# Optimization experiments

Measured on AMD Instinct MI355X. Metric: run time of the kernel, lower is better.

## Reference

```python
import jax, jax.numpy as jnp
import numpy as np

E = 262144   # num edges
T = 1048576  # num triplets
H = 128      # hidden_channels
IE = 64      # int_emb_size
NR = 6       # num_radial
NS = 7       # num_spherical
BD = 8       # basis_emb_size_dist
BA = 8       # basis_emb_size_angle


def setup_inputs() -> dict:
    key = jax.random.key(0)
    ks = jax.random.split(key, 32)
    def rnd(k, shape, s=0.1):
        return jax.random.normal(k, shape, dtype=jnp.float32) * s
    return {
        "x1": rnd(ks[0], (T, H), 1.0),
        "x_old": rnd(ks[1], (E, H), 1.0),
        "rbf0": rnd(ks[2], (E, NR), 1.0),
        "sbf": rnd(ks[3], (T, NS * NR), 1.0),
        "idx_kj": jax.random.randint(ks[4], (T,), 0, E),
        "idx_ji": jax.random.randint(ks[5], (T,), 0, E),
        "W_rbf1": rnd(ks[6], (NR, BD)),
        "W_rbf2": rnd(ks[7], (BD, H)),
        "W_sbf1": rnd(ks[8], (NS * NR, BA)),
        "W_sbf2": rnd(ks[9], (BA, IE)),
        "W_rbf": rnd(ks[10], (NR, H)),
        "W_kj": rnd(ks[11], (H, H)), "b_kj": rnd(ks[12], (H,)),
        "W_ji": rnd(ks[13], (H, H)), "b_ji": rnd(ks[14], (H,)),
        "W_connect": rnd(ks[15], (H, H)), "b_connect": rnd(ks[16], (H,)),
        "W_get_up": rnd(ks[17], (H, H)), "b_get_up": rnd(ks[18], (H,)),
        "W_down": rnd(ks[19], (H, IE)), "b_down": rnd(ks[20], (IE,)),
        "W_up": rnd(ks[21], (IE, H)), "b_up": rnd(ks[22], (H,)),
        "res_before_W": rnd(ks[23], (1, 2, H, H)), "res_before_b": rnd(ks[24], (1, 2, H)),
        "W_lin": rnd(ks[25], (H, H)), "b_lin": rnd(ks[26], (H,)),
        "res_after_W": rnd(ks[27], (2, 2, H, H)), "res_after_b": rnd(ks[28], (2, 2, H)),
    }


def _residual(x, W, b):
    # x + act(lin2(act(lin1(x))))
    h = jax.nn.silu(x @ W[0] + b[0])
    return x + jax.nn.silu(h @ W[1] + b[1])


def reference(x1, x_old, rbf0, sbf, idx_kj, idx_ji, W_rbf1, W_rbf2, W_sbf1, W_sbf2,
              W_rbf, W_kj, b_kj, W_ji, b_ji, W_connect, b_connect, W_get_up, b_get_up,
              W_down, b_down, W_up, b_up, res_before_W, res_before_b, W_lin, b_lin,
              res_after_W, res_after_b):
    act = jax.nn.silu  # swish
    nE = x_old.shape[0]
    # aggregate plane features onto edges
    x_up = jax.ops.segment_sum(x1, idx_ji, num_segments=nE)
    x_up = act(x_up @ W_get_up + b_get_up)
    x_ji = act(x_old @ W_ji + b_ji)
    x_kj = act(x_old @ W_kj + b_kj)
    rbf = (rbf0 @ W_rbf1) @ W_rbf2            # [E, H]
    x_kj = x_kj * rbf
    x_kj = act(x_kj @ W_down + b_down)        # [E, IE]
    sbf_p = (sbf @ W_sbf1) @ W_sbf2           # [T, IE]
    x_kj = x_kj[idx_kj] * sbf_p               # gather edges -> triplets
    x_kj = jax.ops.segment_sum(x_kj, idx_ji, num_segments=nE)  # scatter back to edges
    x_kj = act(x_kj @ W_up + b_up)
    e1 = x_ji + x_kj
    e1 = act(e1 @ W_connect + b_connect) + x_up
    for i in range(res_before_W.shape[0]):
        e1 = _residual(e1, res_before_W[i], res_before_b[i])
    e1 = act(e1 @ W_lin + b_lin) + x_old
    for i in range(res_after_W.shape[0]):
        e1 = _residual(e1, res_after_W[i], res_after_b[i])
    e2 = (rbf0 @ W_rbf) * e1
    return (e1, e2)
```

## Files before the change

### kernel.cpp

```cpp
#include <hip/hip_runtime.h>

#define E_N 262144
#define T_N 1048576

typedef short  bf16x8  __attribute__((ext_vector_type(8)));
typedef short  bf16x4v __attribute__((ext_vector_type(4)));
typedef float  f32x4   __attribute__((ext_vector_type(4)));

#define OFF_KJ    0
#define OFF_DOWN  16384
#define OFF_UP    24576
#define OFF_JI    32768
#define OFF_GU    49152
#define OFF_CN    65536
#define OFF_RB0   81920
#define OFF_RB1   98304
#define OFF_LIN   114688
#define OFF_RA00  131072
#define OFF_RA01  147456
#define OFF_RA10  163840
#define OFF_RA11  180224
#define OFF_END   196608
#define WREG_BYTES 524288u

#define OFFB_AGG   0u
#define OFFB_XKJ   33554432u
#define OFFB_WREG  67108864u
#define OFFB_CNT   67633152u
#define OFFB_POS   68683776u
#define OFFB_TRI   69732352u
#define OFFB_BS    73926656u
#define OFFB_BP    73927680u

__device__ __forceinline__ float silu_f(float x) { return x / (1.0f + __expf(-x)); }

__device__ __forceinline__ unsigned short f2bf(float f) {
  union { float f; unsigned int u; } v; v.f = f;
  unsigned int u = v.u;
  return (unsigned short)((u + 0x7fffu + ((u >> 16) & 1u)) >> 16);
}
__device__ __forceinline__ float bf2f(unsigned short h) {
  union { unsigned int u; float f; } v; v.u = ((unsigned int)h) << 16;
  return v.f;
}

template<int NC>
__device__ __forceinline__ void stage_tile(const float* __restrict__ g, char* __restrict__ lds) {
  constexpr int RB = NC * 2;
  constexpr int C4 = NC / 4;
  for (int i = threadIdx.x; i < 64 * C4; i += 512) {
    int r = i / C4, c4 = i % C4;
    float4 v = *(const float4*)(g + (size_t)r * NC + c4 * 4);
    bf16x4v h;
    h[0] = (short)f2bf(v.x); h[1] = (short)f2bf(v.y);
    h[2] = (short)f2bf(v.z); h[3] = (short)f2bf(v.w);
    *(bf16x4v*)(lds + r * RB + ((c4 * 8) ^ ((r & 7) << 4))) = h;
  }
}

__device__ __forceinline__ void stage_tile_bf16_64(const unsigned short* __restrict__ g,
                                                   char* __restrict__ lds) {
  int i = threadIdx.x;
  int r = i >> 3, c = i & 7;
  int4 v = *(const int4*)((const char*)g + r * 128 + c * 16);
  *(int4*)(lds + r * 128 + ((c * 16) ^ ((r & 7) << 4))) = v;
}

template<int MREP, int NREP, int KSTEPS, int RB>
__device__ __forceinline__ void mfma_gemm(const char* __restrict__ lds, int row0, int col0,
                                          const unsigned short* __restrict__ WT, int lane,
                                          f32x4 (&acc)[MREP][NREP]) {
  const int kg = lane >> 4, r15 = lane & 15;
#pragma unroll
  for (int m = 0; m < MREP; ++m)
#pragma unroll
    for (int n = 0; n < NREP; ++n) acc[m][n] = (f32x4){0.f, 0.f, 0.f, 0.f};
#pragma unroll
  for (int kk = 0; kk < KSTEPS; ++kk) {
    bf16x8 a[MREP], bfr[NREP];
#pragma unroll
    for (int m = 0; m < MREP; ++m) {
      int row = row0 + m * 16 + r15;
      a[m] = *(const bf16x8*)(lds + row * RB + ((kk * 64 + kg * 16) ^ ((row & 7) << 4)));
    }
#pragma unroll
    for (int n = 0; n < NREP; ++n) {
      int nc = col0 + n * 16 + r15;
      bfr[n] = *(const bf16x8*)((const short*)WT + nc * (KSTEPS * 32) + kk * 32 + kg * 8);
    }
#pragma unroll
    for (int m = 0; m < MREP; ++m)
#pragma unroll
      for (int n = 0; n < NREP; ++n)
        acc[m][n] = __builtin_amdgcn_mfma_f32_16x16x32_bf16(a[m], bfr[n], acc[m][n], 0, 0, 0);
  }
}

template<int RB>
__device__ __forceinline__ void write_cd(char* __restrict__ lds, int wrow, int wcol, int lane,
                                         const f32x4 (&v)[2][2]) {
  const int kg = lane >> 4, r15 = lane & 15;
#pragma unroll
  for (int m = 0; m < 2; ++m)
#pragma unroll
    for (int n = 0; n < 2; ++n)
#pragma unroll
      for (int r = 0; r < 4; ++r) {
        int row = wrow + m * 16 + kg * 4 + r;
        int col = wcol + n * 16 + r15;
        *(unsigned short*)(lds + row * RB + ((col * 2) ^ ((row & 7) << 4))) = f2bf(v[m][n][r]);
      }
}

__global__ void __launch_bounds__(256) k_prep(
    const float* __restrict__ W_kj, const float* __restrict__ W_down,
    const float* __restrict__ W_up, const float* __restrict__ W_ji,
    const float* __restrict__ W_get_up, const float* __restrict__ W_connect,
    const float* __restrict__ rbW, const float* __restrict__ W_lin,
    const float* __restrict__ raW,
    const float* __restrict__ W_rbf1, const float* __restrict__ W_rbf2,
    unsigned short* __restrict__ wreg) {
  int b = blockIdx.x;
  if (b == 13) {
    float* W12 = (float*)(wreg + OFF_END);
    for (int i = threadIdx.x; i < 768; i += 256) {
      int r = i >> 7, n = i & 127;
      float s = 0.f;
#pragma unroll
      for (int q = 0; q < 8; ++q) s += W_rbf1[r * 8 + q] * W_rbf2[q * 128 + n];
      W12[i] = s;
    }
    return;
  }
  const float* src; int K = 128, N = 128; int off;
  switch (b) {
    case 0:  src = W_kj;          off = OFF_KJ;  break;
    case 1:  src = W_down;        off = OFF_DOWN; N = 64;  break;
    case 2:  src = W_up;          off = OFF_UP;   K = 64;  break;
    case 3:  src = W_ji;          off = OFF_JI;  break;
    case 4:  src = W_get_up;      off = OFF_GU;  break;
    case 5:  src = W_connect;     off = OFF_CN;  break;
    case 6:  src = rbW;           off = OFF_RB0; break;
    case 7:  src = rbW + 16384;   off = OFF_RB1; break;
    case 8:  src = W_lin;         off = OFF_LIN; break;
    case 9:  src = raW;           off = OFF_RA00; break;
    case 10: src = raW + 16384;   off = OFF_RA01; break;
    case 11: src = raW + 32768;   off = OFF_RA10; break;
    default: src = raW + 49152;   off = OFF_RA11; break;
  }
  unsigned short* dst = wreg + off;
  for (int i = threadIdx.x; i < K * N; i += 256) {
    int k = i / N, n = i % N;
    dst[n * K + k] = f2bf(src[i]);
  }
}

__global__ void __launch_bounds__(256) k_hist(const int* __restrict__ idx_ji,
                                              int* __restrict__ counts) {
  int t = blockIdx.x * 256 + threadIdx.x;
  atomicAdd(&counts[idx_ji[t]], 1);
}

__global__ void __launch_bounds__(1024) k_scan1(const int* __restrict__ counts,
                                                int* __restrict__ locpre,
                                                int* __restrict__ bsum) {
  __shared__ int s[1024];
  int i = blockIdx.x * 1024 + threadIdx.x;
  int v = counts[i];
  s[threadIdx.x] = v; __syncthreads();
  for (int o = 1; o < 1024; o <<= 1) {
    int t = (threadIdx.x >= o) ? s[threadIdx.x - o] : 0;
    __syncthreads();
    s[threadIdx.x] += t;
    __syncthreads();
  }
  locpre[i] = s[threadIdx.x] - v;
  if (threadIdx.x == 1023) bsum[blockIdx.x] = s[1023];
}

__global__ void __launch_bounds__(256) k_scan2(const int* __restrict__ bsum,
                                               int* __restrict__ bpre, int* __restrict__ offs) {
  __shared__ int s[256];
  int v = bsum[threadIdx.x];
  s[threadIdx.x] = v; __syncthreads();
  for (int o = 1; o < 256; o <<= 1) {
    int t = (threadIdx.x >= o) ? s[threadIdx.x - o] : 0;
    __syncthreads();
    s[threadIdx.x] += t;
    __syncthreads();
  }
  bpre[threadIdx.x] = s[threadIdx.x] - v;
  if (threadIdx.x == 0) offs[E_N] = T_N;
}

__global__ void __launch_bounds__(1024) k_scan3(const int* __restrict__ locpre,
                                                const int* __restrict__ bpre,
                                                int* __restrict__ offs,
                                                int* __restrict__ pos) {
  int i = blockIdx.x * 1024 + threadIdx.x;
  int v = locpre[i] + bpre[blockIdx.x];
  offs[i] = v;
  pos[i] = v;
}

__global__ void __launch_bounds__(256) k_fill(const int* __restrict__ idx_ji,
                                              int* __restrict__ pos, int* __restrict__ tri) {
  int t = blockIdx.x * 256 + threadIdx.x;
  int e = idx_ji[t];
  int slot = atomicAdd(&pos[e], 1);
  tri[slot] = t;
}

__global__ void __launch_bounds__(256) k_sbfp(const float* __restrict__ sbf,
                                              const float* __restrict__ W_sbf1,
                                              const float* __restrict__ W_sbf2,
                                              unsigned int* __restrict__ sbfp) {
  __shared__ float s_s[8][42];
  __shared__ float s_t8[8][8];
  int t0 = blockIdx.x * 8;
  for (int i = threadIdx.x; i < 8 * 42; i += 256)
    s_s[i / 42][i % 42] = sbf[(size_t)t0 * 42 + i];
  __syncthreads();
  if (threadIdx.x < 64) {
    int w8 = threadIdx.x >> 3, bb = threadIdx.x & 7;
    float s = 0.f;
#pragma unroll
    for (int r = 0; r < 42; ++r) s += s_s[w8][r] * W_sbf1[r * 8 + bb];
    s_t8[w8][bb] = s;
  }
  __syncthreads();
  int w8 = threadIdx.x >> 5, jj = threadIdx.x & 31;
  float sp0 = 0.f, sp1 = 0.f;
#pragma unroll
  for (int bb = 0; bb < 8; ++bb) {
    float tv = s_t8[w8][bb];
    sp0 += tv * W_sbf2[bb * 64 + jj * 2];
    sp1 += tv * W_sbf2[bb * 64 + jj * 2 + 1];
  }
  unsigned int u = (unsigned int)f2bf(sp0) | ((unsigned int)f2bf(sp1) << 16);
  sbfp[(size_t)(t0 + w8) * 32 + jj] = u;
}

__global__ void __launch_bounds__(256) k_aggB(const int* __restrict__ offs,
                                              const int* __restrict__ tri,
                                              const int* __restrict__ idx_kj,
                                              const unsigned int* __restrict__ sbfp,
                                              const unsigned int* __restrict__ xkj,
                                              unsigned int* __restrict__ agg) {
  int sub = threadIdx.x >> 5, jj = threadIdx.x & 31;
  int e = blockIdx.x * 8 + sub;
  int o0 = offs[e], o1 = offs[e + 1];
  float a0 = 0.f, a1 = 0.f;
  for (int i = o0; i < o1; ++i) {
    int t = tri[i];
    int kj = idx_kj[t];
    unsigned int sv = sbfp[(size_t)t * 32 + jj];
    unsigned int xv = xkj[(size_t)kj * 32 + jj];
    a0 += bf2f((unsigned short)(sv & 0xffff)) * bf2f((unsigned short)(xv & 0xffff));
    a1 += bf2f((unsigned short)(sv >> 16)) * bf2f((unsigned short)(xv >> 16));
  }
  agg[(size_t)e * 32 + jj] = (unsigned int)f2bf(a0) | ((unsigned int)f2bf(a1) << 16);
}

__global__ void __launch_bounds__(256) k_xupg(const int* __restrict__ offs,
                                              const int* __restrict__ tri,
                                              const float* __restrict__ x1,
                                              float* __restrict__ out) {
  int sub = threadIdx.x >> 6, h2 = threadIdx.x & 63;
  int e = blockIdx.x * 4 + sub;
  int o0 = offs[e], o1 = offs[e + 1];
  float a0 = 0.f, a1 = 0.f;
  for (int i = o0; i < o1; ++i) {
    int t = tri[i];
    float2 v = *(const float2*)(x1 + (size_t)t * 128 + h2 * 2);
    a0 += v.x; a1 += v.y;
  }
  *(float2*)(out + (size_t)e * 128 + h2 * 2) = make_float2(a0, a1);
}

__global__ void __launch_bounds__(512, 4) phaseA(
    const float* __restrict__ x_old, const float* __restrict__ rbf0,
    const unsigned short* __restrict__ wreg,
    const float* __restrict__ b_kj, const float* __restrict__ b_down,
    unsigned short* __restrict__ xkjdown) {
  __shared__ char lds[32768];
  char* B0 = lds;
  char* B1 = lds + 16384;
  const int tid = threadIdx.x, lane = tid & 63, wave = tid >> 6;
  const int kg = lane >> 4, r15 = lane & 15;
  const int wrow = (wave >> 2) * 32, wcol = (wave & 3) * 32;
  const size_t e_base = (size_t)blockIdx.x * 64;
  const float* W12 = (const float*)(wreg + OFF_END);

  stage_tile<128>(x_old + e_base * 128, B0);
  __syncthreads();

  f32x4 acc[2][2], val[2][2];
  mfma_gemm<2, 2, 4, 256>(B0, wrow, wcol, wreg + OFF_KJ, lane, acc);
#pragma unroll
  for (int n = 0; n < 2; ++n) {
    int col = wcol + n * 16 + r15;
    float bk = b_kj[col];
    float wc[6];
#pragma unroll
    for (int q = 0; q < 6; ++q) wc[q] = W12[q * 128 + col];
#pragma unroll
    for (int m = 0; m < 2; ++m)
#pragma unroll
      for (int r = 0; r < 4; ++r) {
        int row = wrow + m * 16 + kg * 4 + r;
        const float* rp = rbf0 + (e_base + row) * 6;
        float rv = rp[0]*wc[0] + rp[1]*wc[1] + rp[2]*wc[2] + rp[3]*wc[3] + rp[4]*wc[4] + rp[5]*wc[5];
        val[m][n][r] = silu_f(acc[m][n][r] + bk) * rv;
      }
  }
  __syncthreads();
  write_cd<256>(B1, wrow, wcol, lane, val);
  __syncthreads();

  const int wrow2 = (wave >> 1) * 16, wcol2 = (wave & 1) * 32;
  f32x4 a2[1][2];
  mfma_gemm<1, 2, 4, 256>(B1, wrow2, wcol2, wreg + OFF_DOWN, lane, a2);
#pragma unroll
  for (int n = 0; n < 2; ++n) {
    int col = wcol2 + n * 16 + r15;
    float bd = b_down[col];
#pragma unroll
    for (int r = 0; r < 4; ++r) {
      int row = wrow2 + kg * 4 + r;
      xkjdown[(e_base + row) * 64 + col] = f2bf(silu_f(a2[0][n][r] + bd));
    }
  }
}

__global__ void __launch_bounds__(512, 4) phaseC1(
    const float* __restrict__ x_old, float* __restrict__ e1buf,
    const unsigned short* __restrict__ agg, const unsigned short* __restrict__ wreg,
    const float* __restrict__ b_up, const float* __restrict__ b_ji,
    const float* __restrict__ b_get_up, const float* __restrict__ b_connect,
    const float* __restrict__ rbB, const float* __restrict__ b_lin,
    const float* __restrict__ raB,
    const float* __restrict__ rbf0, const float* __restrict__ W_rbf,
    float* __restrict__ e2o) {
  __shared__ char lds[32768];
  char* B0 = lds;
  char* B1 = lds + 16384;
  const int tid = threadIdx.x, lane = tid & 63, wave = tid >> 6;
  const int kg = lane >> 4, r15 = lane & 15;
  const int wrow = (wave >> 2) * 32, wcol = (wave & 3) * 32;
  const size_t e_base = (size_t)blockIdx.x * 64;

  stage_tile_bf16_64(agg + e_base * 64, B0);
  stage_tile<128>(x_old + e_base * 128, B1);
  __syncthreads();

  f32x4 acc[2][2], acc2[2][2], keep[2][2], tmp[2][2];

  mfma_gemm<2, 2, 2, 128>(B0, wrow, wcol, wreg + OFF_UP, lane, acc);
  mfma_gemm<2, 2, 4, 256>(B1, wrow, wcol, wreg + OFF_JI, lane, acc2);
#pragma unroll
  for (int n = 0; n < 2; ++n) {
    int col = wcol + n * 16 + r15;
    float bu = b_up[col], bj = b_ji[col];
#pragma unroll
    for (int m = 0; m < 2; ++m)
#pragma unroll
      for (int r = 0; r < 4; ++r)
        keep[m][n][r] = silu_f(acc2[m][n][r] + bj) + silu_f(acc[m][n][r] + bu);
  }
  __syncthreads();
  write_cd<256>(B0, wrow, wcol, lane, keep);
  stage_tile<128>(e1buf + e_base * 128, B1);
  __syncthreads();

  mfma_gemm<2, 2, 4, 256>(B1, wrow, wcol, wreg + OFF_GU, lane, acc);
  mfma_gemm<2, 2, 4, 256>(B0, wrow, wcol, wreg + OFF_CN, lane, acc2);
#pragma unroll
  for (int n = 0; n < 2; ++n) {
    int col = wcol + n * 16 + r15;
    float bg = b_get_up[col], bc = b_connect[col];
#pragma unroll
    for (int m = 0; m < 2; ++m)
#pragma unroll
      for (int r = 0; r < 4; ++r)
        keep[m][n][r] = silu_f(acc2[m][n][r] + bc) + silu_f(acc[m][n][r] + bg);
  }
  __syncthreads();
  write_cd<256>(B1, wrow, wcol, lane, keep);
  __syncthreads();

  mfma_gemm<2, 2, 4, 256>(B1, wrow, wcol, wreg + OFF_RB0, lane, acc);
#pragma unroll
  for (int n = 0; n < 2; ++n) {
    float b0v = rbB[wcol + n * 16 + r15];
#pragma unroll
    for (int m = 0; m < 2; ++m)
#pragma unroll
      for (int r = 0; r < 4; ++r) tmp[m][n][r] = silu_f(acc[m][n][r] + b0v);
  }
  __syncthreads();
  write_cd<256>(B0, wrow, wcol, lane, tmp);
  __syncthreads();

  mfma_gemm<2, 2, 4, 256>(B0, wrow, wcol, wreg + OFF_RB1, lane, acc);
#pragma unroll
  for (int n = 0; n < 2; ++n) {
    float b1v = rbB[128 + wcol + n * 16 + r15];
#pragma unroll
    for (int m = 0; m < 2; ++m)
#pragma unroll
      for (int r = 0; r < 4; ++r) keep[m][n][r] += silu_f(acc[m][n][r] + b1v);
  }
  __syncthreads();
  write_cd<256>(B1, wrow, wcol, lane, keep);
  __syncthreads();

  mfma_gemm<2, 2, 4, 256>(B1, wrow, wcol, wreg + OFF_LIN, lane, acc);
#pragma unroll
  for (int n = 0; n < 2; ++n) {
    int col = wcol + n * 16 + r15;
    float bl = b_lin[col];
#pragma unroll
    for (int m = 0; m < 2; ++m)
#pragma unroll
      for (int r = 0; r < 4; ++r) {
        int row = wrow + m * 16 + kg * 4 + r;
        keep[m][n][r] = silu_f(acc[m][n][r] + bl) + x_old[(e_base + row) * 128 + col];
      }
  }
  __syncthreads();
  write_cd<256>(B0, wrow, wcol, lane, keep);
  __syncthreads();

  mfma_gemm<2, 2, 4, 256>(B0, wrow, wcol, wreg + OFF_RA00, lane, acc);
#pragma unroll
  for (int n = 0; n < 2; ++n) {
    float bv = raB[wcol + n * 16 + r15];
#pragma unroll
    for (int m = 0; m < 2; ++m)
#pragma unroll
      for (int r = 0; r < 4; ++r) tmp[m][n][r] = silu_f(acc[m][n][r] + bv);
  }
  __syncthreads();
  write_cd<256>(B1, wrow, wcol, lane, tmp);
  __syncthreads();

  mfma_gemm<2, 2, 4, 256>(B1, wrow, wcol, wreg + OFF_RA01, lane, acc);
#pragma unroll
  for (int n = 0; n < 2; ++n) {
    float bv = raB[128 + wcol + n * 16 + r15];
#pragma unroll
    for (int m = 0; m < 2; ++m)
#pragma unroll
      for (int r = 0; r < 4; ++r) keep[m][n][r] += silu_f(acc[m][n][r] + bv);
  }
  __syncthreads();
  write_cd<256>(B0, wrow, wcol, lane, keep);
  __syncthreads();

  mfma_gemm<2, 2, 4, 256>(B0, wrow, wcol, wreg + OFF_RA10, lane, acc);
#pragma unroll
  for (int n = 0; n < 2; ++n) {
    float bv = raB[256 + wcol + n * 16 + r15];
#pragma unroll
    for (int m = 0; m < 2; ++m)
#pragma unroll
      for (int r = 0; r < 4; ++r) tmp[m][n][r] = silu_f(acc[m][n][r] + bv);
  }
  __syncthreads();
  write_cd<256>(B1, wrow, wcol, lane, tmp);
  __syncthreads();

  mfma_gemm<2, 2, 4, 256>(B1, wrow, wcol, wreg + OFF_RA11, lane, acc);
#pragma unroll
  for (int n = 0; n < 2; ++n) {
    int col = wcol + n * 16 + r15;
    float bv = raB[384 + col];
    float wc[6];
#pragma unroll
    for (int q = 0; q < 6; ++q) wc[q] = W_rbf[q * 128 + col];
#pragma unroll
    for (int m = 0; m < 2; ++m)
#pragma unroll
      for (int r = 0; r < 4; ++r) {
        int row = wrow + m * 16 + kg * 4 + r;
        size_t e = e_base + row;
        float val = keep[m][n][r] + silu_f(acc[m][n][r] + bv);
        e1buf[e * 128 + col] = val;
        if (e2o) {
          const float* rp = rbf0 + e * 6;
          float rv = rp[0]*wc[0] + rp[1]*wc[1] + rp[2]*wc[2] + rp[3]*wc[3] + rp[4]*wc[4] + rp[5]*wc[5];
          e2o[e * 128 + col] = val * rv;
        }
      }
  }
}

__global__ void __launch_bounds__(256) k_e2(const float* __restrict__ e1,
                                            const float* __restrict__ rbf0,
                                            const float* __restrict__ W_rbf,
                                            float* __restrict__ e2) {
  size_t gid = (size_t)blockIdx.x * 256 + threadIdx.x;
  int e = (int)(gid >> 5);
  int c = (int)(gid & 31) << 2;
  float r6[6];
#pragma unroll
  for (int r = 0; r < 6; ++r) r6[r] = rbf0[(size_t)e * 6 + r];
  float4 v = *(const float4*)(e1 + (size_t)e * 128 + c);
  float4 o;
  float rv;
  rv = 0.f;
#pragma unroll
  for (int r = 0; r < 6; ++r) rv += r6[r] * W_rbf[r * 128 + c + 0];
  o.x = v.x * rv;
  rv = 0.f;
#pragma unroll
  for (int r = 0; r < 6; ++r) rv += r6[r] * W_rbf[r * 128 + c + 1];
  o.y = v.y * rv;
  rv = 0.f;
#pragma unroll
  for (int r = 0; r < 6; ++r) rv += r6[r] * W_rbf[r * 128 + c + 2];
  o.z = v.z * rv;
  rv = 0.f;
#pragma unroll
  for (int r = 0; r < 6; ++r) rv += r6[r] * W_rbf[r * 128 + c + 3];
  o.w = v.w * rv;
  *(float4*)(e2 + (size_t)e * 128 + c) = o;
}

extern "C" void kernel_launch(void* const* d_in, const int* in_sizes, int n_in,
                              void* d_out, int out_size, void* d_ws, size_t ws_size,
                              hipStream_t stream) {
  const float* x1        = (const float*)d_in[0];
  const float* x_old     = (const float*)d_in[1];
  const float* rbf0      = (const float*)d_in[2];
  const float* sbf       = (const float*)d_in[3];
  const int*   idx_kj    = (const int*)d_in[4];
  const int*   idx_ji    = (const int*)d_in[5];
  const float* W_rbf1    = (const float*)d_in[6];
  const float* W_rbf2    = (const float*)d_in[7];
  const float* W_sbf1    = (const float*)d_in[8];
  const float* W_sbf2    = (const float*)d_in[9];
  const float* W_rbf     = (const float*)d_in[10];
  const float* W_kj      = (const float*)d_in[11];
  const float* b_kj      = (const float*)d_in[12];
  const float* W_ji      = (const float*)d_in[13];
  const float* b_ji      = (const float*)d_in[14];
  const float* W_connect = (const float*)d_in[15];
  const float* b_connect = (const float*)d_in[16];
  const float* W_get_up  = (const float*)d_in[17];
  const float* b_get_up  = (const float*)d_in[18];
  const float* W_down    = (const float*)d_in[19];
  const float* b_down    = (const float*)d_in[20];
  const float* W_up      = (const float*)d_in[21];
  const float* b_up      = (const float*)d_in[22];
  const float* rbW       = (const float*)d_in[23];
  const float* rbB       = (const float*)d_in[24];
  const float* W_lin     = (const float*)d_in[25];
  const float* b_lin     = (const float*)d_in[26];
  const float* raW       = (const float*)d_in[27];
  const float* raB       = (const float*)d_in[28];

  float* e1buf = (float*)d_out;
  char*  base2 = (char*)d_out + (size_t)E_N * 128 * 4;
  float* e2out = (float*)base2;

  unsigned short* xkj_b = (unsigned short*)(base2 + OFFB_XKJ);
  int* counts = (int*)(base2 + OFFB_CNT);
  int* pos    = (int*)(base2 + OFFB_POS);
  int* tri    = (int*)(base2 + OFFB_TRI);
  int* bsum   = (int*)(base2 + OFFB_BS);
  int* bpre   = (int*)(base2 + OFFB_BP);

  const size_t need_ws = (size_t)WREG_BYTES + (size_t)E_N * 64 * 2;
  const bool fuse = ws_size >= need_ws;
  unsigned short* wreg  = fuse ? (unsigned short*)d_ws
                               : (unsigned short*)(base2 + OFFB_WREG);
  unsigned short* agg_b = fuse ? (unsigned short*)((char*)d_ws + WREG_BYTES)
                               : (unsigned short*)(base2 + OFFB_AGG);

  unsigned int* sbfp_u = (unsigned int*)e1buf;

  k_prep<<<14, 256, 0, stream>>>(W_kj, W_down, W_up, W_ji, W_get_up, W_connect,
                                 rbW, W_lin, raW, W_rbf1, W_rbf2, wreg);

  hipMemsetAsync(counts, 0, (E_N + 1) * sizeof(int), stream);
  k_hist<<<T_N / 256, 256, 0, stream>>>(idx_ji, counts);
  k_scan1<<<256, 1024, 0, stream>>>(counts, pos, bsum);
  k_scan2<<<1, 256, 0, stream>>>(bsum, bpre, counts);
  k_scan3<<<256, 1024, 0, stream>>>(pos, bpre, counts, pos);
  k_fill<<<T_N / 256, 256, 0, stream>>>(idx_ji, pos, tri);

  k_sbfp<<<T_N / 8, 256, 0, stream>>>(sbf, W_sbf1, W_sbf2, sbfp_u);

  phaseA<<<E_N / 64, 512, 0, stream>>>(x_old, rbf0, wreg, b_kj, b_down, xkj_b);

  k_aggB<<<E_N / 8, 256, 0, stream>>>(counts, tri, idx_kj, sbfp_u,
                                      (const unsigned int*)xkj_b, (unsigned int*)agg_b);

  k_xupg<<<E_N / 4, 256, 0, stream>>>(counts, tri, x1, e1buf);

  phaseC1<<<E_N / 64, 512, 0, stream>>>(x_old, e1buf, agg_b, wreg,
                                        b_up, b_ji, b_get_up, b_connect, rbB, b_lin, raB,
                                        rbf0, W_rbf, fuse ? e2out : nullptr);
  if (!fuse)
    k_e2<<<E_N * 32 / 256, 256, 0, stream>>>(e1buf, rbf0, W_rbf, e2out);
}
```

Before: 1.356 ms.

## Restructure edge MLP chain as per-wave register-resident transposed GEMMs

Replaces the 512-thread phaseC1 kernel with phaseC2, in which each wave owns 16 edges and computes every layer as W^T·X^T. Activations stay in registers and are repacked to bf16 through a small per-wave LDS scratch area, so the block-wide __syncthreads between layers go away. Weights are read straight from global memory as MFMA A operands instead of being staged, and bf16 conversion uses v_cvt_pk_bf16_f32. Weight reads now go through cache on every layer, and register pressure rises with 8 fragments of keep and h.

```diff
diff --git a/kernel.cpp b/kernel.cpp
--- a/kernel.cpp
+++ b/kernel.cpp
@@ -34,6 +34,13 @@
 
 __device__ __forceinline__ float silu_f(float x) { return x / (1.0f + __expf(-x)); }
 
+__device__ __forceinline__ f32x4 silu4(f32x4 v) {
+  f32x4 r;
+#pragma unroll
+  for (int i = 0; i < 4; ++i) r[i] = silu_f(v[i]);
+  return r;
+}
+
 __device__ __forceinline__ unsigned short f2bf(float f) {
   union { float f; unsigned int u; } v; v.f = f;
   unsigned int u = v.u;
@@ -42,6 +49,19 @@
 __device__ __forceinline__ float bf2f(unsigned short h) {
   union { unsigned int u; float f; } v; v.u = ((unsigned int)h) << 16;
   return v.f;
+}
+
+__device__ __forceinline__ unsigned cvtpk(float lo, float hi) {
+  unsigned r;
+  asm("v_cvt_pk_bf16_f32 %0, %1, %2" : "=v"(r) : "v"(lo), "v"(hi));
+  return r;
+}
+
+__device__ __forceinline__ bf16x8 pack8(f32x4 a, f32x4 b) {
+  union { bf16x8 v; unsigned u[4]; } t;
+  t.u[0] = cvtpk(a[0], a[1]); t.u[1] = cvtpk(a[2], a[3]);
+  t.u[2] = cvtpk(b[0], b[1]); t.u[3] = cvtpk(b[2], b[3]);
+  return t.v;
 }
 
 template<int NC>
@@ -56,14 +76,6 @@
     h[2] = (short)f2bf(v.z); h[3] = (short)f2bf(v.w);
     *(bf16x4v*)(lds + r * RB + ((c4 * 8) ^ ((r & 7) << 4))) = h;
   }
-}
-
-__device__ __forceinline__ void stage_tile_bf16_64(const unsigned short* __restrict__ g,
-                                                   char* __restrict__ lds) {
-  int i = threadIdx.x;
-  int r = i >> 3, c = i & 7;
-  int4 v = *(const int4*)((const char*)g + r * 128 + c * 16);
-  *(int4*)(lds + r * 128 + ((c * 16) ^ ((r & 7) << 4))) = v;
 }
 
 template<int MREP, int NREP, int KSTEPS, int RB>
@@ -333,7 +345,40 @@
   }
 }
 
-__global__ void __launch_bounds__(512, 4) phaseC1(
+
+__device__ __forceinline__ void repack(const f32x4 (&v)[8], char* __restrict__ rowp,
+                                       int kg, int sw, bf16x8 (&B)[4]) {
+  asm volatile("s_waitcnt lgkmcnt(0)" ::: "memory");
+#pragma unroll
+  for (int f = 0; f < 8; ++f) {
+    uint2 u;
+    u.x = cvtpk(v[f][0], v[f][1]);
+    u.y = cvtpk(v[f][2], v[f][3]);
+    *(uint2*)(rowp + ((f * 32 + kg * 8) ^ sw)) = u;
+  }
+  asm volatile("s_waitcnt lgkmcnt(0)" ::: "memory");
+  __builtin_amdgcn_sched_barrier(0);
+#pragma unroll
+  for (int kk = 0; kk < 4; ++kk)
+    B[kk] = *(const bf16x8*)(rowp + ((kk * 64 + kg * 16) ^ sw));
+}
+
+#define BIAS4(p) (*(const f32x4*)((p) + f * 16 + kg * 4))
+
+#define GEMM8(WTp, KS, BARR, ...)                                                   \
+  _Pragma("unroll")                                                                 \
+  for (int f = 0; f < 8; ++f) {                                                     \
+    f32x4 acc = {0.f, 0.f, 0.f, 0.f};                                               \
+    const unsigned short* Ar = (WTp) + (size_t)(f * 16 + r15) * ((KS) * 32) + kg * 8; \
+    _Pragma("unroll")                                                               \
+    for (int kk = 0; kk < (KS); ++kk) {                                             \
+      bf16x8 a_ = *(const bf16x8*)(Ar + kk * 32);                                   \
+      acc = __builtin_amdgcn_mfma_f32_16x16x32_bf16(a_, (BARR)[kk], acc, 0, 0, 0);  \
+    }                                                                               \
+    __VA_ARGS__;                                                                    \
+  }
+
+__global__ void __launch_bounds__(256, 2) phaseC2(
     const float* __restrict__ x_old, float* __restrict__ e1buf,
     const unsigned short* __restrict__ agg, const unsigned short* __restrict__ wreg,
     const float* __restrict__ b_up, const float* __restrict__ b_ji,
@@ -342,158 +387,83 @@
     const float* __restrict__ raB,
     const float* __restrict__ rbf0, const float* __restrict__ W_rbf,
     float* __restrict__ e2o) {
-  __shared__ char lds[32768];
-  char* B0 = lds;
-  char* B1 = lds + 16384;
+  __shared__ char lds[16384];
   const int tid = threadIdx.x, lane = tid & 63, wave = tid >> 6;
-  const int kg = lane >> 4, r15 = lane & 15;
-  const int wrow = (wave >> 2) * 32, wcol = (wave & 3) * 32;
-  const size_t e_base = (size_t)blockIdx.x * 64;
-
-  stage_tile_bf16_64(agg + e_base * 64, B0);
-  stage_tile<128>(x_old + e_base * 128, B1);
-  __syncthreads();
-
-  f32x4 acc[2][2], acc2[2][2], keep[2][2], tmp[2][2];
-
-  mfma_gemm<2, 2, 2, 128>(B0, wrow, wcol, wreg + OFF_UP, lane, acc);
-  mfma_gemm<2, 2, 4, 256>(B1, wrow, wcol, wreg + OFF_JI, lane, acc2);
-#pragma unroll
-  for (int n = 0; n < 2; ++n) {
-    int col = wcol + n * 16 + r15;
-    float bu = b_up[col], bj = b_ji[col];
-#pragma unroll
-    for (int m = 0; m < 2; ++m)
-#pragma unroll
-      for (int r = 0; r < 4; ++r)
-        keep[m][n][r] = silu_f(acc2[m][n][r] + bj) + silu_f(acc[m][n][r] + bu);
-  }
-  __syncthreads();
-  write_cd<256>(B0, wrow, wcol, lane, keep);
-  stage_tile<128>(e1buf + e_base * 128, B1);
-  __syncthreads();
-
-  mfma_gemm<2, 2, 4, 256>(B1, wrow, wcol, wreg + OFF_GU, lane, acc);
-  mfma_gemm<2, 2, 4, 256>(B0, wrow, wcol, wreg + OFF_CN, lane, acc2);
-#pragma unroll
-  for (int n = 0; n < 2; ++n) {
-    int col = wcol + n * 16 + r15;
-    float bg = b_get_up[col], bc = b_connect[col];
-#pragma unroll
-    for (int m = 0; m < 2; ++m)
-#pragma unroll
-      for (int r = 0; r < 4; ++r)
-        keep[m][n][r] = silu_f(acc2[m][n][r] + bc) + silu_f(acc[m][n][r] + bg);
-  }
-  __syncthreads();
-  write_cd<256>(B1, wrow, wcol, lane, keep);
-  __syncthreads();
-
-  mfma_gemm<2, 2, 4, 256>(B1, wrow, wcol, wreg + OFF_RB0, lane, acc);
-#pragma unroll
-  for (int n = 0; n < 2; ++n) {
-    float b0v = rbB[wcol + n * 16 + r15];
-#pragma unroll
-    for (int m = 0; m < 2; ++m)
-#pragma unroll
-      for (int r = 0; r < 4; ++r) tmp[m][n][r] = silu_f(acc[m][n][r] + b0v);
-  }
-  __syncthreads();
-  write_cd<256>(B0, wrow, wcol, lane, tmp);
-  __syncthreads();
-
-  mfma_gemm<2, 2, 4, 256>(B0, wrow, wcol, wreg + OFF_RB1, lane, acc);
-#pragma unroll
-  for (int n = 0; n < 2; ++n) {
-    float b1v = rbB[128 + wcol + n * 16 + r15];
-#pragma unroll
-    for (int m = 0; m < 2; ++m)
-#pragma unroll
-      for (int r = 0; r < 4; ++r) keep[m][n][r] += silu_f(acc[m][n][r] + b1v);
-  }
-  __syncthreads();
-  write_cd<256>(B1, wrow, wcol, lane, keep);
-  __syncthreads();
-
-  mfma_gemm<2, 2, 4, 256>(B1, wrow, wcol, wreg + OFF_LIN, lane, acc);
-#pragma unroll
-  for (int n = 0; n < 2; ++n) {
-    int col = wcol + n * 16 + r15;
-    float bl = b_lin[col];
-#pragma unroll
-    for (int m = 0; m < 2; ++m)
-#pragma unroll
-      for (int r = 0; r < 4; ++r) {
-        int row = wrow + m * 16 + kg * 4 + r;
-        keep[m][n][r] = silu_f(acc[m][n][r] + bl) + x_old[(e_base + row) * 128 + col];
+  const int r15 = lane & 15, kg = lane >> 4;
+  char* rowp = lds + wave * 4096 + r15 * 256;
+  const int sw = (r15 & 7) << 4;
+  const int e = blockIdx.x * 64 + wave * 16 + r15;
+  const size_t erow = (size_t)e * 128;
+
+  f32x4 keep[8], h[8];
+  bf16x8 Bf[4];
+
+  bf16x8 Bag[2], Bxo[4];
+#pragma unroll
+  for (int kk = 0; kk < 2; ++kk)
+    Bag[kk] = *(const bf16x8*)(agg + (size_t)e * 64 + kk * 32 + kg * 8);
+#pragma unroll
+  for (int kk = 0; kk < 4; ++kk) {
+    f32x4 p = *(const f32x4*)(x_old + erow + kk * 32 + kg * 8);
+    f32x4 q = *(const f32x4*)(x_old + erow + kk * 32 + kg * 8 + 4);
+    Bxo[kk] = pack8(p, q);
+  }
+
+  GEMM8(wreg + OFF_UP, 2, Bag, h[f] = silu4(acc + BIAS4(b_up)))
+  GEMM8(wreg + OFF_JI, 4, Bxo, keep[f] = silu4(acc + BIAS4(b_ji)) + h[f])
+
+  bf16x8 Bxu[4];
+#pragma unroll
+  for (int kk = 0; kk < 4; ++kk) {
+    f32x4 p = *(const f32x4*)(e1buf + erow + kk * 32 + kg * 8);
+    f32x4 q = *(const f32x4*)(e1buf + erow + kk * 32 + kg * 8 + 4);
+    Bxu[kk] = pack8(p, q);
+  }
+  GEMM8(wreg + OFF_GU, 4, Bxu, h[f] = silu4(acc + BIAS4(b_get_up)))
+
+  repack(keep, rowp, kg, sw, Bf);
+  GEMM8(wreg + OFF_CN, 4, Bf, keep[f] = silu4(acc + BIAS4(b_connect)) + h[f])
+
+  repack(keep, rowp, kg, sw, Bf);
+  GEMM8(wreg + OFF_RB0, 4, Bf, h[f] = silu4(acc + BIAS4(rbB)))
+  repack(h, rowp, kg, sw, Bf);
+  GEMM8(wreg + OFF_RB1, 4, Bf, keep[f] = keep[f] + silu4(acc + BIAS4(rbB + 128)))
+
+  repack(keep, rowp, kg, sw, Bf);
+  GEMM8(wreg + OFF_LIN, 4, Bf,
+        keep[f] = silu4(acc + BIAS4(b_lin)) + *(const f32x4*)(x_old + erow + f * 16 + kg * 4))
+
+  repack(keep, rowp, kg, sw, Bf);
+  GEMM8(wreg + OFF_RA00, 4, Bf, h[f] = silu4(acc + BIAS4(raB)))
+  repack(h, rowp, kg, sw, Bf);
+  GEMM8(wreg + OFF_RA01, 4, Bf, keep[f] = keep[f] + silu4(acc + BIAS4(raB + 128)))
+
+  repack(keep, rowp, kg, sw, Bf);
+  GEMM8(wreg + OFF_RA10, 4, Bf, h[f] = silu4(acc + BIAS4(raB + 256)))
+
+  repack(h, rowp, kg, sw, Bf);
+  float r6[6];
+  if (e2o) {
+#pragma unroll
+    for (int q = 0; q < 6; ++q) r6[q] = rbf0[(size_t)e * 6 + q];
+  }
+  GEMM8(wreg + OFF_RA11, 4, Bf, {
+    f32x4 val = keep[f] + silu4(acc + BIAS4(raB + 384));
+    *(f32x4*)(e1buf + erow + f * 16 + kg * 4) = val;
+    if (e2o) {
+      f32x4 rv = {0.f, 0.f, 0.f, 0.f};
+      _Pragma("unroll")
+      for (int q = 0; q < 6; ++q) {
+        f32x4 w = *(const f32x4*)(W_rbf + q * 128 + f * 16 + kg * 4);
+        rv[0] += r6[q] * w[0]; rv[1] += r6[q] * w[1];
+        rv[2] += r6[q] * w[2]; rv[3] += r6[q] * w[3];
       }
-  }
-  __syncthreads();
-  write_cd<256>(B0, wrow, wcol, lane, keep);
-  __syncthreads();
-
-  mfma_gemm<2, 2, 4, 256>(B0, wrow, wcol, wreg + OFF_RA00, lane, acc);
-#pragma unroll
-  for (int n = 0; n < 2; ++n) {
-    float bv = raB[wcol + n * 16 + r15];
-#pragma unroll
-    for (int m = 0; m < 2; ++m)
-#pragma unroll
-      for (int r = 0; r < 4; ++r) tmp[m][n][r] = silu_f(acc[m][n][r] + bv);
-  }
-  __syncthreads();
-  write_cd<256>(B1, wrow, wcol, lane, tmp);
-  __syncthreads();
-
-  mfma_gemm<2, 2, 4, 256>(B1, wrow, wcol, wreg + OFF_RA01, lane, acc);
-#pragma unroll
-  for (int n = 0; n < 2; ++n) {
-    float bv = raB[128 + wcol + n * 16 + r15];
-#pragma unroll
-    for (int m = 0; m < 2; ++m)
-#pragma unroll
-      for (int r = 0; r < 4; ++r) keep[m][n][r] += silu_f(acc[m][n][r] + bv);
-  }
-  __syncthreads();
-  write_cd<256>(B0, wrow, wcol, lane, keep);
-  __syncthreads();
-
-  mfma_gemm<2, 2, 4, 256>(B0, wrow, wcol, wreg + OFF_RA10, lane, acc);
-#pragma unroll
-  for (int n = 0; n < 2; ++n) {
-    float bv = raB[256 + wcol + n * 16 + r15];
-#pragma unroll
-    for (int m = 0; m < 2; ++m)
-#pragma unroll
-      for (int r = 0; r < 4; ++r) tmp[m][n][r] = silu_f(acc[m][n][r] + bv);
-  }
-  __syncthreads();
-  write_cd<256>(B1, wrow, wcol, lane, tmp);
-  __syncthreads();
-
-  mfma_gemm<2, 2, 4, 256>(B1, wrow, wcol, wreg + OFF_RA11, lane, acc);
-#pragma unroll
-  for (int n = 0; n < 2; ++n) {
-    int col = wcol + n * 16 + r15;
-    float bv = raB[384 + col];
-    float wc[6];
-#pragma unroll
-    for (int q = 0; q < 6; ++q) wc[q] = W_rbf[q * 128 + col];
-#pragma unroll
-    for (int m = 0; m < 2; ++m)
-#pragma unroll
-      for (int r = 0; r < 4; ++r) {
-        int row = wrow + m * 16 + kg * 4 + r;
-        size_t e = e_base + row;
-        float val = keep[m][n][r] + silu_f(acc[m][n][r] + bv);
-        e1buf[e * 128 + col] = val;
-        if (e2o) {
-          const float* rp = rbf0 + e * 6;
-          float rv = rp[0]*wc[0] + rp[1]*wc[1] + rp[2]*wc[2] + rp[3]*wc[3] + rp[4]*wc[4] + rp[5]*wc[5];
-          e2o[e * 128 + col] = val * rv;
-        }
-      }
-  }
+      f32x4 o;
+      o[0] = val[0] * rv[0]; o[1] = val[1] * rv[1];
+      o[2] = val[2] * rv[2]; o[3] = val[3] * rv[3];
+      *(f32x4*)(e2o + erow + f * 16 + kg * 4) = o;
+    }
+  })
 }
 
 __global__ void __launch_bounds__(256) k_e2(const float* __restrict__ e1,
@@ -600,7 +570,7 @@
 
   k_xupg<<<E_N / 4, 256, 0, stream>>>(counts, tri, x1, e1buf);
 
-  phaseC1<<<E_N / 64, 512, 0, stream>>>(x_old, e1buf, agg_b, wreg,
+  phaseC2<<<E_N / 64, 256, 0, stream>>>(x_old, e1buf, agg_b, wreg,
                                         b_up, b_ji, b_get_up, b_connect, rbB, b_lin, raB,
                                         rbf0, W_rbf, fuse ? e2out : nullptr);
   if (!fuse)
```

Result: slower. 1.592 ms (+17.4%).
